# Kernel tuning notes

Hardware: AMD Instinct MI355X
Metric: run time of the kernel (lower is better)

Reference implementation:

```python
import jax, jax.numpy as jnp
import numpy as np

NUM_LEVEL = 4

def setup_inputs() -> dict:
    key = jax.random.key(0)
    k1, k2, k3, k4, k5 = jax.random.split(key, 5)
    B, L1, L2, F, H = 8, 1024, 1024, 1024, 1024
    x1_att = jax.random.normal(k1, (B, L1, F), dtype=jnp.float32)
    x2_att = jax.random.normal(k2, (B, L2, F), dtype=jnp.float32)
    x2 = jax.random.normal(k3, (B, L2, H), dtype=jnp.float32)
    x2_mask = jax.random.uniform(k4, (B, L2)) < 0.1
    x2_mask = x2_mask.at[:, 0].set(False)
    W = jax.random.normal(k5, (H, F), dtype=jnp.float32) * 0.02  # nn.Linear weight [out,in]
    final_v = jnp.ones((1, H), dtype=jnp.float32)  # linear_final parameter
    return {"x1_att": x1_att, "x2_att": x2_att, "x2": x2, "x2_mask": x2_mask, "W": W, "final_v": final_v}

def reference(x1_att, x2_att, x2, x2_mask, W, final_v):
    B, L1, F = x1_att.shape
    L2 = x2_att.shape[1]
    H = W.shape[0]
    nl = NUM_LEVEL
    d = H // nl
    # shared linear projection + ReLU (dropout is identity at p=0 / eval)
    x1_key = jax.nn.relu(jnp.einsum('blf,hf->blh', x1_att, W))            # [B,L1,H]
    x2_key = jax.nn.relu(jnp.einsum('blf,hf->blh', x2_att, W)) * final_v  # [B,L2,H]
    x1_rep = x1_key.reshape(B, L1, nl, d)
    x2_rep = x2_key.reshape(B, L2, nl, d)
    # per-level QK^T scores: [B, nl, L1, L2]
    scores = jnp.einsum('bimd,bjmd->bmij', x1_rep, x2_rep)
    scores = jnp.where(x2_mask[:, None, None, :], -jnp.inf, scores)
    alpha = jax.nn.softmax(scores, axis=-1)
    v = x2.reshape(B, L2, nl, d)
    out = jnp.einsum('bmij,bjmd->bimd', alpha, v)  # [B,L1,nl,d]
    return out.reshape(B, L1, H)
```

## Files before the change

### kernel.cpp

```cpp
#include <hip/hip_runtime.h>
#include <hip/hip_bf16.h>
#include <stdint.h>

typedef unsigned short u16;
typedef _Float16 f16_t;
typedef f16_t f16x8 __attribute__((ext_vector_type(8)));
typedef u16 u16x8 __attribute__((ext_vector_type(8)));
typedef u16 u16x4 __attribute__((ext_vector_type(4)));
typedef float f32x4 __attribute__((ext_vector_type(4)));

#define L2E 1.44269504088896f
#define DEFER_THR 7.0f

__device__ __forceinline__ u16 f2h(float f) {
  f16_t h = (f16_t)f;
  return __builtin_bit_cast(u16, h);
}
__device__ __forceinline__ f32x4 mfma16h(u16x8 a, u16x8 b, f32x4 c) {
  return __builtin_amdgcn_mfma_f32_16x16x32_f16(
      __builtin_bit_cast(f16x8, a), __builtin_bit_cast(f16x8, b), c, 0, 0, 0);
}

__global__ void prep_mask_kernel(const unsigned char *__restrict__ mraw,
                                 float *__restrict__ bias) {
  __shared__ int flag;
  int t = threadIdx.x;
  if (t == 0) flag = 0;
  __syncthreads();
  int local = 0;
  for (int i = t; i < 8192; i += 256)
    if ((i & 3) && mraw[i]) local = 1;
  if (local) atomicOr(&flag, 1);
  __syncthreads();
  const bool bytes = (flag != 0);
  const int *mi = (const int *)mraw;
  for (int i = t; i < 8192; i += 256) {
    int m = bytes ? (int)mraw[i] : mi[i];
    bias[i] = m ? -1e30f : 0.0f;
  }
}

__global__ void cvt_f16_kernel(const float *__restrict__ in,
                               u16 *__restrict__ out) {
  int i = (blockIdx.x * 256 + threadIdx.x) * 8;
  f32x4 a = *(const f32x4 *)(in + i);
  f32x4 b = *(const f32x4 *)(in + i + 4);
  u16x8 o;
#pragma unroll
  for (int e = 0; e < 4; ++e) {
    o[e] = f2h(a[e]);
    o[4 + e] = f2h(b[e]);
  }
  *(u16x8 *)(out + i) = o;
}

__global__ void transpose_v_kernel(const float *__restrict__ x2,
                                   u16 *__restrict__ vT) {
  __shared__ float tile[32][33];
  const int b = blockIdx.z, h0 = blockIdx.y * 32, j0 = blockIdx.x * 32;
  const int tx = threadIdx.x & 31, ty = threadIdx.x >> 5;
#pragma unroll
  for (int rr = 0; rr < 32; rr += 8)
    tile[ty + rr][tx] = x2[((size_t)b * 1024 + j0 + ty + rr) * 1024 + h0 + tx];
  __syncthreads();
  const int mlev = h0 >> 8, dd0 = h0 & 255;
#pragma unroll
  for (int rr = 0; rr < 32; rr += 8) {
    int dd = dd0 + ty + rr;
    vT[((size_t)(b * 4 + mlev) * 256 + dd) * 1024 + j0 + tx] =
        f2h(tile[tx][ty + rr]);
  }
}

__global__ __launch_bounds__(256, 2) void proj_kernel(
    const u16 *__restrict__ Ag, const u16 *__restrict__ Bg,
    const float *__restrict__ fv, u16 *__restrict__ outk, int usefv) {
  __shared__ u16 As[128 * 40], Bs[128 * 40];
  const int t = threadIdx.x;
  const int lane = t & 63, wid = t >> 6;
  const int l16 = lane & 15, g = lane >> 4;
  const int wr = wid >> 1, wc = wid & 1;
  const int bm = blockIdx.x, bn = blockIdx.y;

  f32x4 acc[4][4] = {};

  const int srow = t >> 1, c0 = (t & 1) * 16;
  const u16 *aS = Ag + (size_t)(bm * 128 + srow) * 1024 + c0;
  const u16 *bS = Bg + (size_t)(bn * 128 + srow) * 1024 + c0;
  const uint32_t off0 = srow * 80 + c0 * 2, off1 = off0 + 16;

  u16x8 ra0 = *(const u16x8 *)(aS), ra1 = *(const u16x8 *)(aS + 8);
  u16x8 rb0 = *(const u16x8 *)(bS), rb1 = *(const u16x8 *)(bS + 8);

  for (int k0 = 0; k0 < 1024; k0 += 32) {
    __syncthreads();
    *(u16x8 *)((char *)As + off0) = ra0;
    *(u16x8 *)((char *)As + off1) = ra1;
    *(u16x8 *)((char *)Bs + off0) = rb0;
    *(u16x8 *)((char *)Bs + off1) = rb1;
    __syncthreads();
    if (k0 + 32 < 1024) {
      ra0 = *(const u16x8 *)(aS + k0 + 32);
      ra1 = *(const u16x8 *)(aS + k0 + 40);
      rb0 = *(const u16x8 *)(bS + k0 + 32);
      rb1 = *(const u16x8 *)(bS + k0 + 40);
    }

    u16x8 af[4], bf[4];
#pragma unroll
    for (int mf = 0; mf < 4; ++mf) {
      int r = wr * 64 + mf * 16 + l16;
      af[mf] = *(const u16x8 *)((const char *)As + r * 80 + g * 16);
    }
#pragma unroll
    for (int nf = 0; nf < 4; ++nf) {
      int r = wc * 64 + nf * 16 + l16;
      bf[nf] = *(const u16x8 *)((const char *)Bs + r * 80 + g * 16);
    }
    __builtin_amdgcn_s_setprio(1);
#pragma unroll
    for (int mf = 0; mf < 4; ++mf)
#pragma unroll
      for (int nf = 0; nf < 4; ++nf)
        acc[mf][nf] = mfma16h(af[mf], bf[nf], acc[mf][nf]);
    __builtin_amdgcn_s_setprio(0);
  }

#pragma unroll
  for (int nf = 0; nf < 4; ++nf) {
    int col = bn * 128 + wc * 64 + nf * 16 + l16;
    float f = usefv ? fv[col] : 1.0f;
#pragma unroll
    for (int mf = 0; mf < 4; ++mf) {
      int row0 = bm * 128 + wr * 64 + mf * 16 + g * 4;
#pragma unroll
      for (int q = 0; q < 4; ++q) {
        float v = acc[mf][nf][q];
        v = (v > 0.f ? v : 0.f) * f;
        outk[(size_t)(row0 + q) * 1024 + col] = f2h(v);
      }
    }
  }
}

__global__ __launch_bounds__(256, 2) void attn_kernel(
    const u16 *__restrict__ x1k, const u16 *__restrict__ x2k,
    const u16 *__restrict__ vT, const float *__restrict__ bias,
    float *__restrict__ out) {
  __shared__ u16 K2s[32 * 256];
  __shared__ u16 VTs[256 * 32];
  __shared__ float biasS[1024];
  __shared__ u16 P[4][16 * 36];

  const int t = threadIdx.x;
  const int lane = t & 63, wid = t >> 6;
  const int l16 = lane & 15, g = lane >> 4;
  const int id = blockIdx.x;
  const int xcd = id & 7, idx = id >> 3;
  const int it = idx & 15, pp = idx >> 4;
  const int pair = xcd + 8 * pp;
  const int b = pair >> 2, m = pair & 3;

  for (int j = t; j < 1024; j += 256) biasS[j] = bias[b * 1024 + j];

  const int qrow = it * 64 + wid * 16 + l16;
  const u16 *qsrc = x1k + ((size_t)b * 1024 + qrow) * 1024 + m * 256;
  u16x8 Q[8];
#pragma unroll
  for (int dk = 0; dk < 8; ++dk) Q[dk] = *(const u16x8 *)(qsrc + dk * 32 + g * 8);

  f32x4 acc[16] = {};
  float mrow[4] = {-1e30f, -1e30f, -1e30f, -1e30f};
  float lrow[4] = {0.f, 0.f, 0.f, 0.f};

  const int sj = t >> 3;
  const u16 *ksrc = x2k + ((size_t)b * 1024 + sj) * 1024 + m * 256 + (t & 7) * 32;
  const u16 *vtsrc = vT + ((size_t)((b * 4 + m) * 256 + t)) * 1024;
  uint32_t koff[4], voff[4];
#pragma unroll
  for (int q = 0; q < 4; ++q) {
    koff[q] = sj * 512 + ((((t & 7) * 64) + q * 16) ^ ((sj & 7) << 4));
    voff[q] = t * 64 + ((q * 16) ^ ((t & 3) << 4));
  }

  u16x8 pk[4], pv[4];
#pragma unroll
  for (int q = 0; q < 4; ++q) {
    pk[q] = *(const u16x8 *)(ksrc + q * 8);
    pv[q] = *(const u16x8 *)(vtsrc + q * 8);
  }

  for (int jt = 0; jt < 32; ++jt) {
    const int j0 = jt * 32;
    __syncthreads();
#pragma unroll
    for (int q = 0; q < 4; ++q) {
      *(u16x8 *)((char *)K2s + koff[q]) = pk[q];
      *(u16x8 *)((char *)VTs + voff[q]) = pv[q];
    }
    __syncthreads();
    if (jt < 31) {
      const u16 *k2 = ksrc + (size_t)(jt + 1) * 32 * 1024;
      const u16 *v2 = vtsrc + (jt + 1) * 32;
#pragma unroll
      for (int q = 0; q < 4; ++q) {
        pk[q] = *(const u16x8 *)(k2 + q * 8);
        pv[q] = *(const u16x8 *)(v2 + q * 8);
      }
    }

    f32x4 s0 = {0.f, 0.f, 0.f, 0.f}, s1 = {0.f, 0.f, 0.f, 0.f};
    __builtin_amdgcn_s_setprio(1);
    {
      const int j = l16;
      const uint32_t kxo = ((j & 7) << 4);
      const char *row = (const char *)K2s + j * 512;
#pragma unroll
      for (int dk = 0; dk < 8; ++dk) {
        u16x8 kk = *(const u16x8 *)(row + ((uint32_t)(dk * 64 + g * 16) ^ kxo));
        s0 = mfma16h(Q[dk], kk, s0);
      }
    }
    {
      const int j = 16 + l16;
      const uint32_t kxo = ((j & 7) << 4);
      const char *row = (const char *)K2s + j * 512;
#pragma unroll
      for (int dk = 0; dk < 8; ++dk) {
        u16x8 kk = *(const u16x8 *)(row + ((uint32_t)(dk * 64 + g * 16) ^ kxo));
        s1 = mfma16h(Q[dk], kk, s1);
      }
    }
    __builtin_amdgcn_s_setprio(0);

    float sv0[4], sv1[4], tm[4];
    const float bj0 = biasS[j0 + l16], bj1 = biasS[j0 + 16 + l16];
#pragma unroll
    for (int r = 0; r < 4; ++r) {
      sv0[r] = s0[r] + bj0;
      sv1[r] = s1[r] + bj1;
      tm[r] = fmaxf(sv0[r], sv1[r]);
    }
#pragma unroll
    for (int d = 1; d < 16; d <<= 1)
#pragma unroll
      for (int r = 0; r < 4; ++r) tm[r] = fmaxf(tm[r], __shfl_xor(tm[r], d, 64));
    bool need = false;
#pragma unroll
    for (int r = 0; r < 4; ++r)
      need = need || ((tm[r] - mrow[r]) * L2E > DEFER_THR);
    if (__any((int)need)) {
#pragma unroll
      for (int r = 0; r < 4; ++r) {
        float nm = fmaxf(mrow[r], tm[r]);
        float sc = exp2f((mrow[r] - nm) * L2E);
        mrow[r] = nm;
        lrow[r] *= sc;
#pragma unroll
        for (int nf = 0; nf < 16; ++nf) acc[nf][r] *= sc;
      }
    }
    float p0[4], p1[4], rs[4];
#pragma unroll
    for (int r = 0; r < 4; ++r) {
      p0[r] = exp2f((sv0[r] - mrow[r]) * L2E);
      p1[r] = exp2f((sv1[r] - mrow[r]) * L2E);
      rs[r] = p0[r] + p1[r];
    }
#pragma unroll
    for (int d = 1; d < 16; d <<= 1)
#pragma unroll
      for (int r = 0; r < 4; ++r) rs[r] += __shfl_xor(rs[r], d, 64);
#pragma unroll
    for (int r = 0; r < 4; ++r) lrow[r] += rs[r];

    u16 *Pw = &P[wid][0];
#pragma unroll
    for (int r = 0; r < 4; ++r) {
      int il = g * 4 + r;
      Pw[il * 36 + l16] = f2h(p0[r]);
      Pw[il * 36 + 16 + l16] = f2h(p1[r]);
    }
    u16x8 pa;
    {
      const u16 *pp2 = Pw + l16 * 36 + g * 8;
      u16x4 a0 = *(const u16x4 *)(pp2);
      u16x4 a1 = *(const u16x4 *)(pp2 + 4);
      pa = __builtin_shufflevector(a0, a1, 0, 1, 2, 3, 4, 5, 6, 7);
    }
    __builtin_amdgcn_s_setprio(1);
#pragma unroll
    for (int nf = 0; nf < 16; ++nf) {
      int dd = nf * 16 + l16;
      uint32_t off = dd * 64 + ((g * 16) ^ ((dd & 3) << 4));
      u16x8 bb = *(const u16x8 *)((const char *)VTs + off);
      acc[nf] = mfma16h(pa, bb, acc[nf]);
    }
    __builtin_amdgcn_s_setprio(0);
  }

  float inv[4];
#pragma unroll
  for (int r = 0; r < 4; ++r) inv[r] = 1.0f / lrow[r];
#pragma unroll
  for (int nf = 0; nf < 16; ++nf) {
    int col = m * 256 + nf * 16 + l16;
#pragma unroll
    for (int r = 0; r < 4; ++r) {
      int row = it * 64 + wid * 16 + g * 4 + r;
      out[((size_t)b * 1024 + row) * 1024 + col] = acc[nf][r] * inv[r];
    }
  }
}

extern "C" void kernel_launch(void *const *d_in, const int *in_sizes, int n_in,
                              void *d_out, int out_size, void *d_ws,
                              size_t ws_size, hipStream_t stream) {
  const float *x1_att = (const float *)d_in[0];
  const float *x2_att = (const float *)d_in[1];
  const float *x2 = (const float *)d_in[2];
  const unsigned char *mask = (const unsigned char *)d_in[3];
  const float *W = (const float *)d_in[4];
  const float *fv = (const float *)d_in[5];
  float *out = (float *)d_out;

  const size_t MB = 1u << 20;
  char *ws = (char *)d_ws;
  u16 *x1a16 = (u16 *)(ws + 0 * MB);
  u16 *x2a16 = (u16 *)(ws + 16 * MB);
  u16 *W16 = (u16 *)(ws + 32 * MB);
  u16 *x1k = (u16 *)(ws + 34 * MB);
  u16 *x2k = (u16 *)(ws + 50 * MB);
  u16 *vT = (u16 *)(ws + 66 * MB);
  float *bias = (float *)(ws + 82 * MB);

  prep_mask_kernel<<<dim3(1), dim3(256), 0, stream>>>(mask, bias);
  cvt_f16_kernel<<<dim3(4096), dim3(256), 0, stream>>>(x1_att, x1a16);
  cvt_f16_kernel<<<dim3(4096), dim3(256), 0, stream>>>(x2_att, x2a16);
  cvt_f16_kernel<<<dim3(512), dim3(256), 0, stream>>>(W, W16);
  proj_kernel<<<dim3(64, 8), dim3(256), 0, stream>>>(x1a16, W16, fv, x1k, 0);
  proj_kernel<<<dim3(64, 8), dim3(256), 0, stream>>>(x2a16, W16, fv, x2k, 1);
  transpose_v_kernel<<<dim3(32, 32, 8), dim3(256), 0, stream>>>(x2, vT);
  attn_kernel<<<dim3(512), dim3(256), 0, stream>>>(x1k, x2k, vT, bias, out);
}
```

Measured before the change: 326.1 us.

## Use async global-to-LDS double buffering in projection and 64-wide key tiles in attention

The projection GEMM now loads A/B tiles directly into a double-buffered, XOR-swizzled LDS with global_load_lds and explicit vmcnt waits, replacing the register-staged single buffer with two syncthreads per step. The attention kernel processes 64 keys per iteration instead of 32, halving the number of barriers and softmax reductions per key and doubling K-depth per PV MFMA chain. In exchange, LDS use and register pressure (8 prefetch vectors each for K and V) go up, which may lower occupancy.

New measurement: 323.5 us. Within noise of the previous version (-0.8%).

```diff
diff --git a/kernel.cpp b/kernel.cpp
--- a/kernel.cpp
+++ b/kernel.cpp
@@ -19,6 +19,11 @@
 __device__ __forceinline__ f32x4 mfma16h(u16x8 a, u16x8 b, f32x4 c) {
   return __builtin_amdgcn_mfma_f32_16x16x32_f16(
       __builtin_bit_cast(f16x8, a), __builtin_bit_cast(f16x8, b), c, 0, 0, 0);
+}
+__device__ __forceinline__ void gl16(const u16 *g, u16 *l) {
+  __builtin_amdgcn_global_load_lds(
+      (const __attribute__((address_space(1))) void *)g,
+      (__attribute__((address_space(3))) void *)l, 16, 0, 0);
 }
 
 __global__ void prep_mask_kernel(const unsigned char *__restrict__ mraw,
@@ -75,7 +80,7 @@
 __global__ __launch_bounds__(256, 2) void proj_kernel(
     const u16 *__restrict__ Ag, const u16 *__restrict__ Bg,
     const float *__restrict__ fv, u16 *__restrict__ outk, int usefv) {
-  __shared__ u16 As[128 * 40], Bs[128 * 40];
+  __shared__ u16 As[2][128 * 32], Bs[2][128 * 32];
   const int t = threadIdx.x;
   const int lane = t & 63, wid = t >> 6;
   const int l16 = lane & 15, g = lane >> 4;
@@ -84,38 +89,45 @@
 
   f32x4 acc[4][4] = {};
 
-  const int srow = t >> 1, c0 = (t & 1) * 16;
-  const u16 *aS = Ag + (size_t)(bm * 128 + srow) * 1024 + c0;
-  const u16 *bS = Bg + (size_t)(bn * 128 + srow) * 1024 + c0;
-  const uint32_t off0 = srow * 80 + c0 * 2, off1 = off0 + 16;
-
-  u16x8 ra0 = *(const u16x8 *)(aS), ra1 = *(const u16x8 *)(aS + 8);
-  u16x8 rb0 = *(const u16x8 *)(bS), rb1 = *(const u16x8 *)(bS + 8);
-
-  for (int k0 = 0; k0 < 1024; k0 += 32) {
-    __syncthreads();
-    *(u16x8 *)((char *)As + off0) = ra0;
-    *(u16x8 *)((char *)As + off1) = ra1;
-    *(u16x8 *)((char *)Bs + off0) = rb0;
-    *(u16x8 *)((char *)Bs + off1) = rb1;
-    __syncthreads();
-    if (k0 + 32 < 1024) {
-      ra0 = *(const u16x8 *)(aS + k0 + 32);
-      ra1 = *(const u16x8 *)(aS + k0 + 40);
-      rb0 = *(const u16x8 *)(bS + k0 + 32);
-      rb1 = *(const u16x8 *)(bS + k0 + 40);
-    }
+  const int rA0 = 32 * wid + (lane >> 2), rA1 = rA0 + 16;
+  const int cA0 = (lane & 3) ^ ((rA0 >> 1) & 3);
+  const int cA1 = (lane & 3) ^ ((rA1 >> 1) & 3);
+  const u16 *srcA0 = Ag + (size_t)(bm * 128 + rA0) * 1024 + cA0 * 8;
+  const u16 *srcA1 = Ag + (size_t)(bm * 128 + rA1) * 1024 + cA1 * 8;
+  const u16 *srcB0 = Bg + (size_t)(bn * 128 + rA0) * 1024 + cA0 * 8;
+  const u16 *srcB1 = Bg + (size_t)(bn * 128 + rA1) * 1024 + cA1 * 8;
+  const int dst0 = wid * 1024, dst1 = wid * 1024 + 512;
+
+  gl16(srcA0, &As[0][dst0]);
+  gl16(srcA1, &As[0][dst1]);
+  gl16(srcB0, &Bs[0][dst0]);
+  gl16(srcB1, &Bs[0][dst1]);
+
+  for (int k0 = 0; k0 < 32; ++k0) {
+    const int cur = k0 & 1;
+    if (k0 < 31) {
+      const int kel = (k0 + 1) * 32, nb = cur ^ 1;
+      gl16(srcA0 + kel, &As[nb][dst0]);
+      gl16(srcA1 + kel, &As[nb][dst1]);
+      gl16(srcB0 + kel, &Bs[nb][dst0]);
+      gl16(srcB1 + kel, &Bs[nb][dst1]);
+      asm volatile("s_waitcnt vmcnt(4)" ::: "memory");
+    } else {
+      asm volatile("s_waitcnt vmcnt(0)" ::: "memory");
+    }
+    __builtin_amdgcn_s_barrier();
+    asm volatile("" ::: "memory");
 
     u16x8 af[4], bf[4];
 #pragma unroll
     for (int mf = 0; mf < 4; ++mf) {
       int r = wr * 64 + mf * 16 + l16;
-      af[mf] = *(const u16x8 *)((const char *)As + r * 80 + g * 16);
+      af[mf] = *(const u16x8 *)(&As[cur][0] + r * 32 + ((g ^ ((r >> 1) & 3)) * 8));
     }
 #pragma unroll
     for (int nf = 0; nf < 4; ++nf) {
       int r = wc * 64 + nf * 16 + l16;
-      bf[nf] = *(const u16x8 *)((const char *)Bs + r * 80 + g * 16);
+      bf[nf] = *(const u16x8 *)(&Bs[cur][0] + r * 32 + ((g ^ ((r >> 1) & 3)) * 8));
     }
     __builtin_amdgcn_s_setprio(1);
 #pragma unroll
@@ -124,6 +136,8 @@
       for (int nf = 0; nf < 4; ++nf)
         acc[mf][nf] = mfma16h(af[mf], bf[nf], acc[mf][nf]);
     __builtin_amdgcn_s_setprio(0);
+    asm volatile("" ::: "memory");
+    __builtin_amdgcn_s_barrier();
   }
 
 #pragma unroll
@@ -147,10 +161,10 @@
     const u16 *__restrict__ x1k, const u16 *__restrict__ x2k,
     const u16 *__restrict__ vT, const float *__restrict__ bias,
     float *__restrict__ out) {
-  __shared__ u16 K2s[32 * 256];
-  __shared__ u16 VTs[256 * 32];
+  __shared__ u16 K2s[64 * 256];
+  __shared__ u16 VTs[256 * 64];
   __shared__ float biasS[1024];
-  __shared__ u16 P[4][16 * 36];
+  __shared__ u16 P[4][16 * 72];
 
   const int t = threadIdx.x;
   const int lane = t & 63, wid = t >> 6;
@@ -173,73 +187,65 @@
   float mrow[4] = {-1e30f, -1e30f, -1e30f, -1e30f};
   float lrow[4] = {0.f, 0.f, 0.f, 0.f};
 
-  const int sj = t >> 3;
-  const u16 *ksrc = x2k + ((size_t)b * 1024 + sj) * 1024 + m * 256 + (t & 7) * 32;
+  const int sj = t >> 2, cb = (t & 3) * 8;
+  const u16 *ksrc = x2k + ((size_t)b * 1024 + sj) * 1024 + m * 256 + cb * 8;
   const u16 *vtsrc = vT + ((size_t)((b * 4 + m) * 256 + t)) * 1024;
-  uint32_t koff[4], voff[4];
-#pragma unroll
-  for (int q = 0; q < 4; ++q) {
-    koff[q] = sj * 512 + ((((t & 7) * 64) + q * 16) ^ ((sj & 7) << 4));
-    voff[q] = t * 64 + ((q * 16) ^ ((t & 3) << 4));
-  }
-
-  u16x8 pk[4], pv[4];
-#pragma unroll
-  for (int q = 0; q < 4; ++q) {
+  uint32_t koff[8], voff[8];
+#pragma unroll
+  for (int q = 0; q < 8; ++q) {
+    koff[q] = sj * 512 + ((uint32_t)((cb + q) ^ (sj & 7)) << 4);
+    voff[q] = t * 128 + ((uint32_t)(q ^ (t & 7)) << 4);
+  }
+
+  u16x8 pk[8], pv[8];
+#pragma unroll
+  for (int q = 0; q < 8; ++q) {
     pk[q] = *(const u16x8 *)(ksrc + q * 8);
     pv[q] = *(const u16x8 *)(vtsrc + q * 8);
   }
 
-  for (int jt = 0; jt < 32; ++jt) {
-    const int j0 = jt * 32;
+  for (int jt = 0; jt < 16; ++jt) {
     __syncthreads();
 #pragma unroll
-    for (int q = 0; q < 4; ++q) {
+    for (int q = 0; q < 8; ++q) {
       *(u16x8 *)((char *)K2s + koff[q]) = pk[q];
       *(u16x8 *)((char *)VTs + voff[q]) = pv[q];
     }
     __syncthreads();
-    if (jt < 31) {
-      const u16 *k2 = ksrc + (size_t)(jt + 1) * 32 * 1024;
-      const u16 *v2 = vtsrc + (jt + 1) * 32;
-#pragma unroll
-      for (int q = 0; q < 4; ++q) {
+    if (jt < 15) {
+      const u16 *k2 = ksrc + (size_t)(jt + 1) * 64 * 1024;
+      const u16 *v2 = vtsrc + (jt + 1) * 64;
+#pragma unroll
+      for (int q = 0; q < 8; ++q) {
         pk[q] = *(const u16x8 *)(k2 + q * 8);
         pv[q] = *(const u16x8 *)(v2 + q * 8);
       }
     }
 
-    f32x4 s0 = {0.f, 0.f, 0.f, 0.f}, s1 = {0.f, 0.f, 0.f, 0.f};
+    f32x4 s[4] = {};
     __builtin_amdgcn_s_setprio(1);
-    {
-      const int j = l16;
-      const uint32_t kxo = ((j & 7) << 4);
-      const char *row = (const char *)K2s + j * 512;
-#pragma unroll
-      for (int dk = 0; dk < 8; ++dk) {
-        u16x8 kk = *(const u16x8 *)(row + ((uint32_t)(dk * 64 + g * 16) ^ kxo));
-        s0 = mfma16h(Q[dk], kk, s0);
-      }
-    }
-    {
-      const int j = 16 + l16;
-      const uint32_t kxo = ((j & 7) << 4);
-      const char *row = (const char *)K2s + j * 512;
-#pragma unroll
-      for (int dk = 0; dk < 8; ++dk) {
-        u16x8 kk = *(const u16x8 *)(row + ((uint32_t)(dk * 64 + g * 16) ^ kxo));
-        s1 = mfma16h(Q[dk], kk, s1);
+#pragma unroll
+    for (int dk = 0; dk < 8; ++dk) {
+#pragma unroll
+      for (int jh = 0; jh < 4; ++jh) {
+        const int j = jh * 16 + l16;
+        uint32_t off = j * 512 + ((uint32_t)((dk * 4 + g) ^ (j & 7)) << 4);
+        u16x8 kk = *(const u16x8 *)((const char *)K2s + off);
+        s[jh] = mfma16h(Q[dk], kk, s[jh]);
       }
     }
     __builtin_amdgcn_s_setprio(0);
 
-    float sv0[4], sv1[4], tm[4];
-    const float bj0 = biasS[j0 + l16], bj1 = biasS[j0 + 16 + l16];
+    const int j0 = jt * 64;
+    float bj[4];
+#pragma unroll
+    for (int jh = 0; jh < 4; ++jh) bj[jh] = biasS[j0 + jh * 16 + l16];
+    float tm[4];
 #pragma unroll
     for (int r = 0; r < 4; ++r) {
-      sv0[r] = s0[r] + bj0;
-      sv1[r] = s1[r] + bj1;
-      tm[r] = fmaxf(sv0[r], sv1[r]);
+#pragma unroll
+      for (int jh = 0; jh < 4; ++jh) s[jh][r] += bj[jh];
+      tm[r] = fmaxf(fmaxf(s[0][r], s[1][r]), fmaxf(s[2][r], s[3][r]));
     }
 #pragma unroll
     for (int d = 1; d < 16; d <<= 1)
@@ -260,12 +266,12 @@
         for (int nf = 0; nf < 16; ++nf) acc[nf][r] *= sc;
       }
     }
-    float p0[4], p1[4], rs[4];
+    float p[4][4], rs[4];
 #pragma unroll
     for (int r = 0; r < 4; ++r) {
-      p0[r] = exp2f((sv0[r] - mrow[r]) * L2E);
-      p1[r] = exp2f((sv1[r] - mrow[r]) * L2E);
-      rs[r] = p0[r] + p1[r];
+#pragma unroll
+      for (int jh = 0; jh < 4; ++jh) p[jh][r] = exp2f((s[jh][r] - mrow[r]) * L2E);
+      rs[r] = (p[0][r] + p[1][r]) + (p[2][r] + p[3][r]);
     }
 #pragma unroll
     for (int d = 1; d < 16; d <<= 1)
@@ -276,25 +282,24 @@
 
     u16 *Pw = &P[wid][0];
 #pragma unroll
-    for (int r = 0; r < 4; ++r) {
-      int il = g * 4 + r;
-      Pw[il * 36 + l16] = f2h(p0[r]);
-      Pw[il * 36 + 16 + l16] = f2h(p1[r]);
-    }
-    u16x8 pa;
-    {
-      const u16 *pp2 = Pw + l16 * 36 + g * 8;
-      u16x4 a0 = *(const u16x4 *)(pp2);
-      u16x4 a1 = *(const u16x4 *)(pp2 + 4);
-      pa = __builtin_shufflevector(a0, a1, 0, 1, 2, 3, 4, 5, 6, 7);
-    }
+    for (int jh = 0; jh < 4; ++jh)
+#pragma unroll
+      for (int r = 0; r < 4; ++r)
+        Pw[(g * 4 + r) * 72 + jh * 16 + l16] = f2h(p[jh][r]);
+    u16x8 pa[2];
+#pragma unroll
+    for (int kk = 0; kk < 2; ++kk)
+      pa[kk] = *(const u16x8 *)(Pw + l16 * 72 + kk * 32 + g * 8);
     __builtin_amdgcn_s_setprio(1);
 #pragma unroll
     for (int nf = 0; nf < 16; ++nf) {
-      int dd = nf * 16 + l16;
-      uint32_t off = dd * 64 + ((g * 16) ^ ((dd & 3) << 4));
-      u16x8 bb = *(const u16x8 *)((const char *)VTs + off);
-      acc[nf] = mfma16h(pa, bb, acc[nf]);
+      const int dd = nf * 16 + l16;
+#pragma unroll
+      for (int kk = 0; kk < 2; ++kk) {
+        uint32_t off = dd * 128 + ((uint32_t)((kk * 4 + g) ^ (dd & 7)) << 4);
+        u16x8 bb = *(const u16x8 *)((const char *)VTs + off);
+        acc[nf] = mfma16h(pa[kk], bb, acc[nf]);
+      }
     }
     __builtin_amdgcn_s_setprio(0);
   }
```
